# Optimization experiments

Measured on AMD Instinct MI355X. Metric: run time of the kernel, lower is better.

## Reference

```python
import jax, jax.numpy as jnp
from jax import lax
import numpy as np

INPUT_POINTS = 4096
NUM_STAGES = 4
EMBED_DIM = 72
K_NEIGHBORS = 90
ALPHA = 1000.0
BETA = 100.0
B = 4
EPS = 1e-5


def pos_embed(coords, out_dim):
    """coords: [B, Cin, *rest] -> [B, out_dim, *rest].
    Matches PosE_Initial/PosE_Geo: sin/cos interleaved along the feature axis."""
    Bsz, cin = coords.shape[0], coords.shape[1]
    rest = coords.shape[2:]
    feat_dim = out_dim // (cin * 2)
    dim_embed = ALPHA ** (jnp.arange(feat_dim, dtype=coords.dtype) / feat_dim)
    div = BETA * coords[..., None] / dim_embed                 # [B,Cin,*rest,f]
    emb = jnp.stack([jnp.sin(div), jnp.cos(div)], axis=-1)      # [B,Cin,*rest,f,2]
    emb = emb.reshape(coords.shape + (2 * feat_dim,))           # interleave sin/cos
    emb = jnp.moveaxis(emb, -1, 2)                              # [B,Cin,2f,*rest]
    return emb.reshape((Bsz, out_dim) + rest)


def fps(points, n):
    """Farthest point sampling, deterministic start at index 0. points [N,3]."""
    d0 = jnp.full(points.shape[0], jnp.inf, dtype=points.dtype)

    def step(carry, _):
        d, last = carry
        dist = jnp.sum((points - points[last]) ** 2, axis=-1)
        d = jnp.minimum(d, dist)
        return (d, jnp.argmax(d)), last

    _, idx = lax.scan(step, (d0, jnp.argmax(jnp.zeros(points.shape[0]))), None, length=n)
    return idx


def gather_points(points, idx):
    # points [B,N,C], idx [B,...] -> [B,...,C]
    return jax.vmap(lambda p, i: p[i])(points, idx)


def knn_indices(xyz, new_xyz, k):
    # squared pairwise distances [B,S,N] then k smallest
    sq = (jnp.sum(new_xyz ** 2, -1)[:, :, None]
          + jnp.sum(xyz ** 2, -1)[:, None, :]
          - 2.0 * jnp.einsum('bsc,bnc->bsn', new_xyz, xyz))
    _, idx = lax.top_k(-sq, k)
    return idx


def stage(xyz, x, group_num, out_dim, gamma, beta_p):
    # xyz [B,N,3], x [B,N,C]
    fi = fps(xyz[0], group_num)                 # shared across batch (fps with batch=None)
    lc_xyz = xyz[:, fi]                         # [B,G,3]
    lc_x = x[:, fi]                             # [B,G,C]
    ki = knn_indices(xyz, lc_xyz, K_NEIGHBORS)  # [B,G,K]
    knn_xyz = gather_points(xyz, ki)            # [B,G,K,3]
    knn_x = gather_points(x, ki)                # [B,G,K,C]
    # LGA: global scalar std (unbiased, like torch.std) normalization
    dx = knn_x - lc_x[:, :, None, :]
    dxyz = knn_xyz - lc_xyz[:, :, None, :]
    knn_xn = dx / (jnp.std(dx, ddof=1) + EPS)
    knn_xyzn = dxyz / (jnp.std(dxyz, ddof=1) + EPS)
    feat = jnp.concatenate(
        [knn_xn, jnp.broadcast_to(lc_x[:, :, None, :], knn_xn.shape)], axis=-1)
    feat = jnp.transpose(feat, (0, 3, 1, 2))                    # [B,out,G,K]
    pe = pos_embed(jnp.transpose(knn_xyzn, (0, 3, 1, 2)), out_dim)
    w = (feat + pe) * pe                                        # [B,out,G,K]
    # Pooling: max+mean over K, BatchNorm1d (training stats), exact GELU
    lc = jnp.max(w, -1) + jnp.mean(w, -1)                       # [B,out,G]
    mu = jnp.mean(lc, axis=(0, 2), keepdims=True)
    var = jnp.var(lc, axis=(0, 2), keepdims=True)
    lc = (lc - mu) / jnp.sqrt(var + EPS) * gamma[None, :, None] + beta_p[None, :, None]
    return lc_xyz, jax.nn.gelu(lc, approximate=False)


def forward(xyz, x, gammas, betas):
    feat = pos_embed(x, EMBED_DIM)              # [B,72,N]
    out_dim = EMBED_DIM
    group = INPUT_POINTS
    for i in range(NUM_STAGES):
        out_dim *= 2
        group //= 2
        xyz, feat = stage(xyz, jnp.transpose(feat, (0, 2, 1)),
                          group, out_dim, gammas[i], betas[i])
    return jnp.max(feat, -1) + jnp.mean(feat, -1)


def setup_inputs() -> dict:
    key = jax.random.key(0)
    k1, k2 = jax.random.split(key)
    inp = {
        'xyz': jax.random.normal(k1, (B, INPUT_POINTS, 3), jnp.float32),
        'x': jax.random.normal(k2, (B, 3, INPUT_POINTS), jnp.float32),
    }
    dims = [EMBED_DIM * 2 ** (i + 1) for i in range(NUM_STAGES)]
    for i, d in enumerate(dims):
        inp[f'gamma{i}'] = jnp.ones((d,), jnp.float32)
        inp[f'beta{i}'] = jnp.zeros((d,), jnp.float32)
    return inp


def reference(xyz, x, gamma0, beta0, gamma1, beta1, gamma2, beta2, gamma3, beta3):
    return forward(xyz, x,
                   [gamma0, gamma1, gamma2, gamma3],
                   [beta0, beta1, beta2, beta3])
```

## Files before the change

### kernel.cpp

```cpp
#include <hip/hip_runtime.h>

typedef unsigned int u32;
typedef unsigned long long u64;
typedef float v2f __attribute__((ext_vector_type(2)));

#define BB 4
#define NP0 4096
#define KNB 90
#define CC0 72
#define MAXD 1152
#define NSTRIPE 16

__global__ void k_init(const float* __restrict__ xyz, const float* __restrict__ x,
                       float* __restrict__ xs, float* __restrict__ ys, float* __restrict__ zs,
                       float* __restrict__ feat, float* __restrict__ sums){
  int i = blockIdx.x*blockDim.x + threadIdx.x;
  if (i < 16) sums[i] = 0.f;
  if (i < BB*NP0){
    xs[i] = xyz[3*i+0];
    ys[i] = xyz[3*i+1];
    zs[i] = xyz[3*i+2];
  }
  if (i < BB*NP0*36){
    int j = i % 36; int bn = i / 36;
    int n = bn % NP0, b = bn / NP0;
    int cin = j / 12, f = j % 12;
    float xv = x[(b*3+cin)*NP0 + n];
    float rcp = __powf(1000.0f, -(float)f / 12.0f);
    float a = (100.0f * xv) * rcp;
    float sn, cs; __sincosf(a, &sn, &cs);
    float2 v = make_float2(sn, cs);
    *(float2*)(feat + (size_t)bn*CC0 + cin*24 + 2*f) = v;
  }
}

__device__ __forceinline__ void wave_argmax(float bd, int bi, float &smax, int &wbi){
  float v = bd;
  #define DPP_MAX(ctrl) do{ int _t = __builtin_amdgcn_mov_dpp(__float_as_int(v), (ctrl), 0xf, 0xf, true); \
                            v = fmaxf(v, __int_as_float(_t)); }while(0)
  DPP_MAX(0x111); DPP_MAX(0x112); DPP_MAX(0x114); DPP_MAX(0x118);
  DPP_MAX(0x142); DPP_MAX(0x143);
  #undef DPP_MAX
  smax = __int_as_float(__builtin_amdgcn_readlane(__float_as_int(v), 63));
  u64 msk = __ballot(bd == smax);
  int winlane = (int)__ffsll((long long)msk) - 1;
  wbi = __builtin_amdgcn_readlane(bi, winlane);
}

template<int PPT>
__global__ __launch_bounds__(256)
void k_fps4(const float* __restrict__ xs, const float* __restrict__ ys, const float* __restrict__ zs,
            int N, int G, int* __restrict__ fi,
            float* __restrict__ nxs, float* __restrict__ nys, float* __restrict__ nzs){
  constexpr int PH = PPT/2;
  __shared__ float4 sp[4096];
  __shared__ int sfi[2048];
  __shared__ u64 cand[2][4];
  int tid = threadIdx.x;
  const int base = tid * PPT;
  int wv = tid >> 6;
  int lane = tid & 63;
  v2f px[PH], py[PH], pz[PH], dmn[PH];
  #pragma unroll
  for (int j=0;j<PH;j++){
    int n = base + 2*j;
    float2 ax = *(const float2*)(xs+n);
    float2 ay = *(const float2*)(ys+n);
    float2 az = *(const float2*)(zs+n);
    px[j] = (v2f){ax.x, ax.y};
    py[j] = (v2f){ay.x, ay.y};
    pz[j] = (v2f){az.x, az.y};
    sp[n]   = make_float4(ax.x, ay.x, az.x, 0.f);
    sp[n+1] = make_float4(ax.y, ay.y, az.y, 0.f);
    dmn[j] = (v2f){INFINITY, INFINITY};
  }
  if (tid==0){ sfi[0]=0; }
  float lx = xs[0], ly = ys[0], lz = zs[0];
  __syncthreads();
  for (int t=1; t<G; t++){
    float bd = -INFINITY; int bi = base;
    v2f lx2 = (v2f){lx,lx}, ly2 = (v2f){ly,ly}, lz2 = (v2f){lz,lz};
    {
      #pragma clang fp contract(off)
      #pragma unroll
      for (int j=0;j<PH;j++){
        v2f dx = px[j] - lx2;
        v2f dy = py[j] - ly2;
        v2f dz = pz[j] - lz2;
        v2f d2 = (dx*dx + dy*dy) + dz*dz;
        v2f dmo = dmn[j];
        float dm0 = fminf(dmo.x, d2.x);
        float dm1 = fminf(dmo.y, d2.y);
        dmn[j] = (v2f){dm0, dm1};
        bool g0 = dm0 > bd;
        bd = g0 ? dm0 : bd;
        bi = g0 ? (base + 2*j) : bi;
        bool g1 = dm1 > bd;
        bd = g1 ? dm1 : bd;
        bi = g1 ? (base + 2*j + 1) : bi;
      }
    }
    float smax; int wbi;
    wave_argmax(bd, bi, smax, wbi);
    int par = t & 1;
    if (lane == 0) cand[par][wv] = ((u64)__float_as_uint(smax) << 32) | (u32)(~(u32)wbi);
    __syncthreads();
    u64 k0 = cand[par][0], k1 = cand[par][1], k2 = cand[par][2], k3 = cand[par][3];
    u64 ka = k0 > k1 ? k0 : k1;
    u64 kb = k2 > k3 ? k2 : k3;
    u64 km = ka > kb ? ka : kb;
    int w = (int)(~(u32)km);
    if ((u32)w >= (u32)N) w = 0;
    float4 p = sp[w];
    lx = p.x; ly = p.y; lz = p.z;
    if (tid==0){ sfi[t] = w; }
  }
  __syncthreads();
  for (int i = tid; i < G; i += 256) fi[i] = sfi[i];
  for (int i = tid; i < BB*G; i += 256){
    int b = i / G, g = i % G;
    int idx = sfi[g];
    nxs[i] = xs[(size_t)b*N + idx];
    nys[i] = ys[(size_t)b*N + idx];
    nzs[i] = zs[(size_t)b*N + idx];
  }
}

__device__ float blockReduceSum(float v, float* sRed){
  for (int off=32; off; off>>=1) v += __shfl_down(v, off, 64);
  int wid = threadIdx.x >> 6, lane = threadIdx.x & 63;
  __syncthreads();
  if (lane==0) sRed[wid] = v;
  __syncthreads();
  float r = 0;
  if (threadIdx.x == 0){ for (int i=0;i<4;i++) r += sRed[i]; }
  return r;
}

template<int C, int NF>
__global__ __launch_bounds__(256)
void k_knnstd(const float* __restrict__ x,
              const float* __restrict__ xs, const float* __restrict__ ys, const float* __restrict__ zs,
              const float* __restrict__ nxs, const float* __restrict__ nys, const float* __restrict__ nzs,
              const int* __restrict__ fi, int N, int G,
              int* __restrict__ ki, float* __restrict__ sums,
              int* __restrict__ fi2, float* __restrict__ n2xs,
              float* __restrict__ n2ys, float* __restrict__ n2zs){
  extern __shared__ u32 smk[];
  __shared__ u64 candF[2][4];
  int tid = threadIdx.x;
  if constexpr (NF > 0){
    if (blockIdx.x == 0){
      constexpr int PPT = NF/256;
      constexpr int PH = PPT/2;
      constexpr int G2 = NF/2;
      float4* sp = (float4*)smk;
      int* sfi = ((int*)smk) + NF*4;
      const int base = tid * PPT;
      int wv = tid >> 6, lane = tid & 63;
      v2f px[PH], py[PH], pz[PH], dmn[PH];
      #pragma unroll
      for (int j=0;j<PH;j++){
        int n = base + 2*j;
        float2 ax = *(const float2*)(nxs+n);
        float2 ay = *(const float2*)(nys+n);
        float2 az = *(const float2*)(nzs+n);
        px[j] = (v2f){ax.x, ax.y};
        py[j] = (v2f){ay.x, ay.y};
        pz[j] = (v2f){az.x, az.y};
        sp[n]   = make_float4(ax.x, ay.x, az.x, 0.f);
        sp[n+1] = make_float4(ax.y, ay.y, az.y, 0.f);
        dmn[j] = (v2f){INFINITY, INFINITY};
      }
      if (tid==0){ sfi[0]=0; }
      float lx = nxs[0], ly = nys[0], lz = nzs[0];
      __syncthreads();
      for (int t=1; t<G2; t++){
        float bd = -INFINITY; int bi = base;
        v2f lx2 = (v2f){lx,lx}, ly2 = (v2f){ly,ly}, lz2 = (v2f){lz,lz};
        {
          #pragma clang fp contract(off)
          #pragma unroll
          for (int j=0;j<PH;j++){
            v2f dx = px[j] - lx2;
            v2f dy = py[j] - ly2;
            v2f dz = pz[j] - lz2;
            v2f d2 = (dx*dx + dy*dy) + dz*dz;
            v2f dmo = dmn[j];
            float dm0 = fminf(dmo.x, d2.x);
            float dm1 = fminf(dmo.y, d2.y);
            dmn[j] = (v2f){dm0, dm1};
            bool g0 = dm0 > bd;
            bd = g0 ? dm0 : bd;
            bi = g0 ? (base + 2*j) : bi;
            bool g1 = dm1 > bd;
            bd = g1 ? dm1 : bd;
            bi = g1 ? (base + 2*j + 1) : bi;
          }
        }
        float smax; int wbi;
        wave_argmax(bd, bi, smax, wbi);
        int par = t & 1;
        if (lane == 0) candF[par][wv] = ((u64)__float_as_uint(smax) << 32) | (u32)(~(u32)wbi);
        __syncthreads();
        u64 k0 = candF[par][0], k1 = candF[par][1], k2 = candF[par][2], k3 = candF[par][3];
        u64 ka = k0 > k1 ? k0 : k1;
        u64 kb = k2 > k3 ? k2 : k3;
        u64 km = ka > kb ? ka : kb;
        int w = (int)(~(u32)km);
        if ((u32)w >= (u32)NF) w = 0;
        float4 p = sp[w];
        lx = p.x; ly = p.y; lz = p.z;
        if (tid==0){ sfi[t] = w; }
      }
      __syncthreads();
      for (int i = tid; i < G2; i += 256) fi2[i] = sfi[i];
      for (int i = tid; i < BB*G2; i += 256){
        int b2 = i / G2, g2 = i % G2;
        int idx = sfi[g2];
        n2xs[i] = nxs[(size_t)b2*G + idx];
        n2ys[i] = nys[(size_t)b2*G + idx];
        n2zs[i] = nzs[(size_t)b2*G + idx];
      }
      return;
    }
  }
  u32* keys = smk;
  u32* hist = smk + N;
  u32* eq   = hist + 256;
  u32* sc   = eq + 512;
  u32* wtot = sc + 4;
  __shared__ float sLcx[C];
  __shared__ int sKi[KNB];
  __shared__ int sFi;
  __shared__ float sRed[4];
  int bid = (NF > 0) ? ((int)blockIdx.x - 1) : (int)blockIdx.x;
  int wv = tid >> 6, lane = tid & 63;
  int g = bid % G, b = bid / G;
  if (tid==0){ int f0 = fi[g]; if ((u32)f0 >= (u32)N) f0 = 0; sFi = f0; }
  float cx = nxs[b*G+g], cy = nys[b*G+g], cz = nzs[b*G+g];
  float ss = __fadd_rn(__fadd_rn(__fmul_rn(cx,cx), __fmul_rn(cy,cy)), __fmul_rn(cz,cz));
  for (int n = tid; n < N; n += 256){
    float px = xs[b*N+n], py = ys[b*N+n], pz = zs[b*N+n];
    float nn  = __fadd_rn(__fadd_rn(__fmul_rn(px,px), __fmul_rn(py,py)), __fmul_rn(pz,pz));
    float dot = __fadd_rn(__fadd_rn(__fmul_rn(cx,px), __fmul_rn(cy,py)), __fmul_rn(cz,pz));
    float sq  = __fsub_rn(__fadd_rn(ss, nn), __fmul_rn(2.0f, dot));
    u32 u = __float_as_uint(sq);
    keys[n] = (u & 0x80000000u) ? ~u : (u | 0x80000000u);
  }
  if (tid < 4) sc[tid] = 0;
  __syncthreads();
  for (int c = tid; c < C; c += 256) sLcx[c] = x[(size_t)(b*N + sFi)*C + c];
  u32 prefix = 0, bas = 0;
  for (int pass=0; pass<4; pass++){
    int shift = 24 - 8*pass;
    u32 mask = (pass==0) ? 0u : (0xFFFFFFFFu << (shift+8));
    hist[tid] = 0;
    __syncthreads();
    for (int n = tid; n < N; n += 256){
      u32 k = keys[n];
      if ((k & mask) == (prefix & mask))
        atomicAdd(&hist[(k >> shift) & 255u], 1u);
    }
    __syncthreads();
    u32 h = hist[tid];
    u32 p = h;
    #pragma unroll
    for (int off=1; off<64; off<<=1){
      u32 o = __shfl_up(p, off, 64);
      if (lane >= off) p += o;
    }
    if (lane == 63) wtot[wv] = p;
    __syncthreads();
    u32 ex = p - h;
    for (int w2=0; w2<wv; w2++) ex += wtot[w2];
    if (bas + ex < KNB && bas + ex + h >= KNB){
      sc[0] = prefix | ((u32)tid << shift);
      sc[1] = bas + ex;
    }
    __syncthreads();
    prefix = sc[0]; bas = sc[1];
    __syncthreads();
  }
  u32 T = prefix;
  int needEq = KNB - (int)bas;
  int* out = ki + (size_t)(b*G+g)*KNB;
  for (int n = tid; n < N; n += 256){
    u32 k = keys[n];
    if (k < T){
      u32 p2 = atomicAdd(&sc[2], 1u);
      if (p2 < KNB){ out[p2] = n; sKi[p2] = n; }
    } else if (k == T){
      u32 e = atomicAdd(&sc[3], 1u);
      if (e < 512) eq[e] = (u32)n;
    }
  }
  __syncthreads();
  int m = (int)sc[3]; if (m > 512) m = 512;
  for (int i = tid; i < m; i += 256){
    u32 v = eq[i];
    int r = 0;
    for (int j=0; j<m; j++) r += (eq[j] < v);
    if (r < needEq){
      u32 p2 = atomicAdd(&sc[2], 1u);
      if (p2 < KNB){ out[p2] = (int)v; sKi[p2] = (int)v; }
    }
  }
  __syncthreads();
  if (tid == 0){
    u32 c = sc[2];
    while (c < KNB){ out[c] = 0; sKi[c] = 0; c++; }
  }
  __syncthreads();
  float s1=0, s2=0, s3=0, s4=0;
  constexpr int C2 = C/2;
  for (int u2 = tid; u2 < KNB*C2; u2 += 256){
    int k = u2 / C2; int c = (u2 - k*C2)*2;
    int idx = sKi[k];
    float2 v = *(const float2*)(x + (size_t)(b*N + idx)*C + c);
    float a0 = v.x - sLcx[c];
    float a1 = v.y - sLcx[c+1];
    s1 += a0 + a1; s2 += a0*a0 + a1*a1;
  }
  if (tid < 3){
    for (int k=0;k<KNB;k++){
      int idx = sKi[k];
      float pc = (tid==0 ? xs[b*N+idx] : tid==1 ? ys[b*N+idx] : zs[b*N+idx]);
      float cc = (tid==0 ? cx : tid==1 ? cy : cz);
      float w = pc - cc;
      s3 += w; s4 += w*w;
    }
  }
  float t;
  t = blockReduceSum(s1, sRed); if (tid==0) atomicAdd(&sums[0], t);
  t = blockReduceSum(s2, sRed); if (tid==0) atomicAdd(&sums[1], t);
  t = blockReduceSum(s3, sRed); if (tid==0) atomicAdd(&sums[2], t);
  t = blockReduceSum(s4, sRed); if (tid==0) atomicAdd(&sums[3], t);
}

template<int C>
__global__ void k_feat(const float* __restrict__ x,
            const float* __restrict__ xs, const float* __restrict__ ys, const float* __restrict__ zs,
            const float* __restrict__ nxs, const float* __restrict__ nys, const float* __restrict__ nzs,
            const int* __restrict__ fi, const int* __restrict__ ki, const float* __restrict__ sums,
            double n1, double n2,
            int N, int G, float* __restrict__ lc){
  constexpr int D = 2*C;
  constexpr int D3 = D/3;
  constexpr int FD = C/3;
  __shared__ float sLcx[C];
  __shared__ float sDx[KNB*3];
  __shared__ int sKi[KNB];
  __shared__ int sFi;
  __shared__ float sC[3];
  __shared__ float sInv2[2];
  int tid = threadIdx.x;
  int g = blockIdx.x % G, b = blockIdx.x / G;
  if (tid==0){ int f0 = fi[g]; if ((u32)f0 >= (u32)N) f0 = 0; sFi = f0; }
  if (tid==0){
    double s1 = sums[0], s2 = sums[1];
    double mean = s1/n1;
    double var = (s2 - s1*mean)/(n1 - 1.0); if (var < 0) var = 0;
    sInv2[0] = (float)(1.0/(sqrt(var) + 1e-5));
    double t1 = sums[2], t2 = sums[3];
    double m2 = t1/n2;
    double v2 = (t2 - t1*m2)/(n2 - 1.0); if (v2 < 0) v2 = 0;
    sInv2[1] = (float)(1.0/(sqrt(v2) + 1e-5));
  }
  if (tid<3) sC[tid] = (tid==0 ? nxs[b*G+g] : tid==1 ? nys[b*G+g] : nzs[b*G+g]);
  if (tid < KNB){ int v = ki[(size_t)(b*G+g)*KNB + tid]; if ((u32)v >= (u32)N) v = 0; sKi[tid] = v; }
  __syncthreads();
  for (int c = tid; c < C; c += blockDim.x) sLcx[c] = x[(size_t)(b*N + sFi)*C + c];
  for (int t = tid; t < KNB*3; t += blockDim.x){
    int k = t/3, c = t%3;
    int idx = sKi[k];
    float pc = (c==0 ? xs[b*N+idx] : c==1 ? ys[b*N+idx] : zs[b*N+idx]);
    sDx[t] = (pc - sC[c]) * sInv2[1];
  }
  __syncthreads();
  int p = tid;
  if (p >= C) return;
  int d0 = 2*p;
  int c = d0 / D3;
  int f = (d0 - c*D3) >> 1;
  float rcp = __powf(1000.0f, -(float)f / (float)FD);
  bool low = (d0 < C);
  float invdx = sInv2[0];
  float fh0 = 0.f, fh1 = 0.f;
  if (!low){ fh0 = sLcx[d0-C]; fh1 = sLcx[d0+1-C]; }
  float l0 = low ? sLcx[d0] : 0.f, l1 = low ? sLcx[d0+1] : 0.f;
  float mx0=-INFINITY, mx1=-INFINITY, sm0=0.f, sm1=0.f;
  for (int k=0;k<KNB;k++){
    float a = (100.0f * sDx[k*3+c]) * rcp;
    float sn, cs; __sincosf(a, &sn, &cs);
    float f0, f1;
    if (low){
      float2 v = *(const float2*)(x + (size_t)(b*N + sKi[k])*C + d0);
      f0 = (v.x - l0) * invdx;
      f1 = (v.y - l1) * invdx;
    } else { f0 = fh0; f1 = fh1; }
    float w0 = (f0 + sn)*sn;
    float w1 = (f1 + cs)*cs;
    mx0 = fmaxf(mx0, w0); sm0 += w0;
    mx1 = fmaxf(mx1, w1); sm1 += w1;
  }
  float* o = lc + (size_t)(b*G+g)*D + d0;
  o[0] = mx0 + sm0/90.0f;
  o[1] = mx1 + sm1/90.0f;
}

__global__ __launch_bounds__(256)
void k_bnpart(const float* __restrict__ lc, int D, int M,
              double* __restrict__ PS, double* __restrict__ PQ){
  __shared__ double sS[4][64], sQ[4][64];
  int lane = threadIdx.x & 63, row = threadIdx.x >> 6;
  int tile = blockIdx.x, stripe = blockIdx.y;
  int d = tile*64 + lane;
  int span = M / NSTRIPE;
  int i0 = stripe * span;
  double s=0, q=0;
  if (d < D){
    for (int i=i0+row; i<i0+span; i+=4){
      float v = lc[(size_t)i*D + d];
      s += v; q += (double)v*v;
    }
  }
  sS[row][lane]=s; sQ[row][lane]=q;
  __syncthreads();
  if (row==0 && d < D){
    PS[(size_t)stripe*MAXD + d] = sS[0][lane]+sS[1][lane]+sS[2][lane]+sS[3][lane];
    PQ[(size_t)stripe*MAXD + d] = sQ[0][lane]+sQ[1][lane]+sQ[2][lane]+sQ[3][lane];
  }
}

__global__ void k_bnfin(const double* __restrict__ PS, const double* __restrict__ PQ,
                        const float* __restrict__ gamma, const float* __restrict__ beta,
                        int D, int M, float* __restrict__ A, float* __restrict__ Bb){
  int d = blockIdx.x*64 + threadIdx.x;
  if (d >= D) return;
  double ts=0, tq=0;
  for (int s=0; s<NSTRIPE; s++){ ts += PS[(size_t)s*MAXD + d]; tq += PQ[(size_t)s*MAXD + d]; }
  double mean = ts / M;
  double var = tq / M - mean*mean; if (var < 0) var = 0;
  float rstd = (float)(1.0/sqrt(var + 1e-5));
  float gm = gamma[d], bt = beta[d];
  A[d] = gm*rstd;
  Bb[d] = bt - (float)mean*gm*rstd;
}

__global__ void k_apply(float* __restrict__ lc, const float* __restrict__ A,
                        const float* __restrict__ Bb, int D, int total){
  int i = blockIdx.x*blockDim.x + threadIdx.x;
  if (i >= total) return;
  int d = i % D;
  float v = lc[i]*A[d] + Bb[d];
  lc[i] = 0.5f * v * (1.0f + erff(v * 0.70710678118654752f));
}

__global__ void k_out(const float* __restrict__ feat, float* __restrict__ out){
  int i = blockIdx.x*blockDim.x + threadIdx.x;
  if (i >= BB*1152) return;
  int b = i / 1152, d = i % 1152;
  const float* base = feat + (size_t)b*256*1152 + d;
  float mx = -INFINITY, sm = 0.f;
  for (int g=0; g<256; g++){
    float v = base[(size_t)g*1152];
    mx = fmaxf(mx, v); sm += v;
  }
  out[i] = mx + sm/256.0f;
}

extern "C" void kernel_launch(void* const* d_in, const int* in_sizes, int n_in,
                              void* d_out, int out_size, void* d_ws, size_t ws_size,
                              hipStream_t stream) {
  const float* xyz = (const float*)d_in[0];
  const float* xin = (const float*)d_in[1];
  float* ws = (float*)d_ws;
  size_t off = 0;
  const size_t PS_ = (size_t)BB*NP0;
  const size_t XS = (size_t)BB*NP0*CC0;
  float* T0[3]; float* T1[3]; float* T2[3];
  for (int i=0;i<3;i++){ T0[i] = ws + off; off += PS_; }
  for (int i=0;i<3;i++){ T1[i] = ws + off; off += PS_; }
  for (int i=0;i<3;i++){ T2[i] = ws + off; off += PS_; }
  float* xA = ws + off; off += XS;
  float* xB = ws + off; off += XS;
  int*   fiA = (int*)(ws + off); off += 2048;
  int*   fiB = (int*)(ws + off); off += 2048;
  int*   ki = (int*)(ws + off); off += (size_t)BB*2048*KNB;
  float* sums = ws + off; off += 16;
  float* Abn  = ws + off; off += 1152;
  float* Bbn  = ws + off; off += 1152;
  off = (off + 1) & ~(size_t)1;
  double* PSb = (double*)(ws + off); off += (size_t)NSTRIPE*MAXD*2;
  double* PQb = (double*)(ws + off); off += (size_t)NSTRIPE*MAXD*2;

  k_init<<<(BB*NP0*36+255)/256, 256, 0, stream>>>(xyz, xin, T0[0], T0[1], T0[2], xA, sums);
  k_fps4<16><<<1, 256, 0, stream>>>(T0[0],T0[1],T0[2], NP0, NP0/2, fiA, T1[0],T1[1],T1[2]);

  float **P = T0, **Cn = T1, **Nx = T2;
  int *fiC = fiA, *fiN = fiB;
  float *xc = xA, *lc = xB;
  for (int s=0; s<4; s++){
    int N = NP0 >> s, G = N >> 1, C = CC0 << s, D = 2*C;
    float* ssum = sums + 4*s;
    size_t knn_need = (size_t)(N + 256 + 512 + 8 + 8)*4;
    if (s==0){
      size_t lds = knn_need; size_t fps_need = (size_t)2048*16 + 1024*4;
      if (fps_need > lds) lds = fps_need;
      k_knnstd<72,2048><<<BB*G+1, 256, lds, stream>>>(xc, P[0],P[1],P[2], Cn[0],Cn[1],Cn[2],
          fiC, N, G, ki, ssum, fiN, Nx[0],Nx[1],Nx[2]);
    } else if (s==1){
      size_t lds = knn_need; size_t fps_need = (size_t)1024*16 + 512*4;
      if (fps_need > lds) lds = fps_need;
      k_knnstd<144,1024><<<BB*G+1, 256, lds, stream>>>(xc, P[0],P[1],P[2], Cn[0],Cn[1],Cn[2],
          fiC, N, G, ki, ssum, fiN, Nx[0],Nx[1],Nx[2]);
    } else if (s==2){
      size_t lds = knn_need; size_t fps_need = (size_t)512*16 + 256*4;
      if (fps_need > lds) lds = fps_need;
      k_knnstd<288,512><<<BB*G+1, 256, lds, stream>>>(xc, P[0],P[1],P[2], Cn[0],Cn[1],Cn[2],
          fiC, N, G, ki, ssum, fiN, Nx[0],Nx[1],Nx[2]);
    } else {
      k_knnstd<576,0><<<BB*G, 256, knn_need, stream>>>(xc, P[0],P[1],P[2], Cn[0],Cn[1],Cn[2],
          fiC, N, G, ki, ssum, nullptr, nullptr, nullptr, nullptr);
    }
    double n1 = (double)BB*G*KNB*C, n2 = (double)BB*G*KNB*3;
    int Tp = ((C + 63)/64)*64;
    if (s==0)      k_feat<72 ><<<BB*G, Tp, 0, stream>>>(xc, P[0],P[1],P[2], Cn[0],Cn[1],Cn[2], fiC, ki, ssum, n1, n2, N, G, lc);
    else if (s==1) k_feat<144><<<BB*G, Tp, 0, stream>>>(xc, P[0],P[1],P[2], Cn[0],Cn[1],Cn[2], fiC, ki, ssum, n1, n2, N, G, lc);
    else if (s==2) k_feat<288><<<BB*G, Tp, 0, stream>>>(xc, P[0],P[1],P[2], Cn[0],Cn[1],Cn[2], fiC, ki, ssum, n1, n2, N, G, lc);
    else           k_feat<576><<<BB*G, Tp, 0, stream>>>(xc, P[0],P[1],P[2], Cn[0],Cn[1],Cn[2], fiC, ki, ssum, n1, n2, N, G, lc);
    int M = BB*G;
    dim3 bng((D + 63)/64, NSTRIPE);
    k_bnpart<<<bng, 256, 0, stream>>>(lc, D, M, PSb, PQb);
    k_bnfin<<<(D + 63)/64, 64, 0, stream>>>(PSb, PQb, (const float*)d_in[2+2*s],
                                            (const float*)d_in[3+2*s], D, M, Abn, Bbn);
    int total = M*D;
    k_apply<<<(total+255)/256, 256, 0, stream>>>(lc, Abn, Bbn, D, total);
    float** t = P; P = Cn; Cn = Nx; Nx = t;
    int* ti = fiC; fiC = fiN; fiN = ti;
    float* tf = xc; xc = lc; lc = tf;
  }
  k_out<<<(BB*1152+255)/256, 256, 0, stream>>>(xc, (float*)d_out);
}
```

Baseline: 2.488 ms.

## Split next-stage FPS across knn and feat kernels with spilled state

Measured after the change: 2.633 ms. 1.06x slower.

```diff
diff --git a/kernel.cpp b/kernel.cpp
--- a/kernel.cpp
+++ b/kernel.cpp
@@ -10,6 +10,7 @@
 #define CC0 72
 #define MAXD 1152
 #define NSTRIPE 16
+#define FSPLIT 700
 
 __global__ void k_init(const float* __restrict__ xyz, const float* __restrict__ x,
                        float* __restrict__ xs, float* __restrict__ ys, float* __restrict__ zs,
@@ -126,6 +127,108 @@
   }
 }
 
+template<int NF, int NT>
+__device__ __forceinline__
+void fps_chunk(const float* __restrict__ cxs, const float* __restrict__ cys, const float* __restrict__ czs,
+               int t0, int t1,
+               float* __restrict__ dmnG, float4* __restrict__ cenG,
+               int* __restrict__ fi2,
+               float* __restrict__ n2xs, float* __restrict__ n2ys, float* __restrict__ n2zs,
+               u64 (&cand)[2][4]){
+  constexpr int PPT = NF/NT;
+  constexpr int PH = PPT/2;
+  constexpr int G2 = NF/2;
+  constexpr int NW = NT/64;
+  int tid = threadIdx.x;
+  const int base = tid * PPT;
+  int wv = tid >> 6, lane = tid & 63;
+  v2f px[PH], py[PH], pz[PH], dmn[PH];
+  #pragma unroll
+  for (int j=0;j<PH;j++){
+    int n = base + 2*j;
+    float2 ax = *(const float2*)(cxs+n);
+    float2 ay = *(const float2*)(cys+n);
+    float2 az = *(const float2*)(czs+n);
+    px[j] = (v2f){ax.x, ax.y};
+    py[j] = (v2f){ay.x, ay.y};
+    pz[j] = (v2f){az.x, az.y};
+  }
+  float lx, ly, lz;
+  if (t0 == 1){
+    #pragma unroll
+    for (int j=0;j<PH;j++) dmn[j] = (v2f){INFINITY, INFINITY};
+    if (tid==0) fi2[0] = 0;
+    lx = cxs[0]; ly = cys[0]; lz = czs[0];
+  } else {
+    #pragma unroll
+    for (int j=0;j<PH;j++){
+      float2 dv = *(const float2*)(dmnG + base + 2*j);
+      dmn[j] = (v2f){dv.x, dv.y};
+    }
+    float4 c = *cenG;
+    lx = c.x; ly = c.y; lz = c.z;
+  }
+  for (int t=t0; t<t1; t++){
+    float bd = -INFINITY; int bi = base;
+    v2f lx2 = (v2f){lx,lx}, ly2 = (v2f){ly,ly}, lz2 = (v2f){lz,lz};
+    {
+      #pragma clang fp contract(off)
+      #pragma unroll
+      for (int j=0;j<PH;j++){
+        v2f dx = px[j] - lx2;
+        v2f dy = py[j] - ly2;
+        v2f dz = pz[j] - lz2;
+        v2f d2 = (dx*dx + dy*dy) + dz*dz;
+        v2f dmo = dmn[j];
+        float dm0 = fminf(dmo.x, d2.x);
+        float dm1 = fminf(dmo.y, d2.y);
+        dmn[j] = (v2f){dm0, dm1};
+        bool g0 = dm0 > bd;
+        bd = g0 ? dm0 : bd;
+        bi = g0 ? (base + 2*j) : bi;
+        bool g1 = dm1 > bd;
+        bd = g1 ? dm1 : bd;
+        bi = g1 ? (base + 2*j + 1) : bi;
+      }
+    }
+    float smax; int wbi;
+    wave_argmax(bd, bi, smax, wbi);
+    int par = t & 1;
+    if (lane == 0) cand[par][wv] = ((u64)__float_as_uint(smax) << 32) | (u32)(~(u32)wbi);
+    __syncthreads();
+    u64 km;
+    if constexpr (NW == 4){
+      u64 k0 = cand[par][0], k1 = cand[par][1], k2 = cand[par][2], k3 = cand[par][3];
+      u64 ka = k0 > k1 ? k0 : k1;
+      u64 kb = k2 > k3 ? k2 : k3;
+      km = ka > kb ? ka : kb;
+    } else {
+      u64 k0 = cand[par][0], k1 = cand[par][1];
+      km = k0 > k1 ? k0 : k1;
+    }
+    int w = (int)(~(u32)km);
+    if ((u32)w >= (u32)NF) w = 0;
+    lx = cxs[w]; ly = cys[w]; lz = czs[w];
+    if (tid==0) fi2[t] = w;
+  }
+  if (t1 < G2){
+    #pragma unroll
+    for (int j=0;j<PH;j++)
+      *(float2*)(dmnG + base + 2*j) = make_float2(dmn[j].x, dmn[j].y);
+    if (tid==0) *cenG = make_float4(lx, ly, lz, 0.f);
+  } else {
+    __syncthreads();
+    for (int i = tid; i < BB*G2; i += NT){
+      int b2 = i / G2, g2 = i % G2;
+      int idx = fi2[g2];
+      if ((u32)idx >= (u32)NF) idx = 0;
+      n2xs[i] = cxs[(size_t)b2*NF + idx];
+      n2ys[i] = cys[(size_t)b2*NF + idx];
+      n2zs[i] = czs[(size_t)b2*NF + idx];
+    }
+  }
+}
+
 __device__ float blockReduceSum(float v, float* sRed){
   for (int off=32; off; off>>=1) v += __shfl_down(v, off, 64);
   int wid = threadIdx.x >> 6, lane = threadIdx.x & 63;
@@ -144,6 +247,7 @@
               const float* __restrict__ nxs, const float* __restrict__ nys, const float* __restrict__ nzs,
               const int* __restrict__ fi, int N, int G,
               int* __restrict__ ki, float* __restrict__ sums,
+              int t0, int t1, float* __restrict__ dmnG, float4* __restrict__ cenG,
               int* __restrict__ fi2, float* __restrict__ n2xs,
               float* __restrict__ n2ys, float* __restrict__ n2zs){
   extern __shared__ u32 smk[];
@@ -151,77 +255,7 @@
   int tid = threadIdx.x;
   if constexpr (NF > 0){
     if (blockIdx.x == 0){
-      constexpr int PPT = NF/256;
-      constexpr int PH = PPT/2;
-      constexpr int G2 = NF/2;
-      float4* sp = (float4*)smk;
-      int* sfi = ((int*)smk) + NF*4;
-      const int base = tid * PPT;
-      int wv = tid >> 6, lane = tid & 63;
-      v2f px[PH], py[PH], pz[PH], dmn[PH];
-      #pragma unroll
-      for (int j=0;j<PH;j++){
-        int n = base + 2*j;
-        float2 ax = *(const float2*)(nxs+n);
-        float2 ay = *(const float2*)(nys+n);
-        float2 az = *(const float2*)(nzs+n);
-        px[j] = (v2f){ax.x, ax.y};
-        py[j] = (v2f){ay.x, ay.y};
-        pz[j] = (v2f){az.x, az.y};
-        sp[n]   = make_float4(ax.x, ay.x, az.x, 0.f);
-        sp[n+1] = make_float4(ax.y, ay.y, az.y, 0.f);
-        dmn[j] = (v2f){INFINITY, INFINITY};
-      }
-      if (tid==0){ sfi[0]=0; }
-      float lx = nxs[0], ly = nys[0], lz = nzs[0];
-      __syncthreads();
-      for (int t=1; t<G2; t++){
-        float bd = -INFINITY; int bi = base;
-        v2f lx2 = (v2f){lx,lx}, ly2 = (v2f){ly,ly}, lz2 = (v2f){lz,lz};
-        {
-          #pragma clang fp contract(off)
-          #pragma unroll
-          for (int j=0;j<PH;j++){
-            v2f dx = px[j] - lx2;
-            v2f dy = py[j] - ly2;
-            v2f dz = pz[j] - lz2;
-            v2f d2 = (dx*dx + dy*dy) + dz*dz;
-            v2f dmo = dmn[j];
-            float dm0 = fminf(dmo.x, d2.x);
-            float dm1 = fminf(dmo.y, d2.y);
-            dmn[j] = (v2f){dm0, dm1};
-            bool g0 = dm0 > bd;
-            bd = g0 ? dm0 : bd;
-            bi = g0 ? (base + 2*j) : bi;
-            bool g1 = dm1 > bd;
-            bd = g1 ? dm1 : bd;
-            bi = g1 ? (base + 2*j + 1) : bi;
-          }
-        }
-        float smax; int wbi;
-        wave_argmax(bd, bi, smax, wbi);
-        int par = t & 1;
-        if (lane == 0) candF[par][wv] = ((u64)__float_as_uint(smax) << 32) | (u32)(~(u32)wbi);
-        __syncthreads();
-        u64 k0 = candF[par][0], k1 = candF[par][1], k2 = candF[par][2], k3 = candF[par][3];
-        u64 ka = k0 > k1 ? k0 : k1;
-        u64 kb = k2 > k3 ? k2 : k3;
-        u64 km = ka > kb ? ka : kb;
-        int w = (int)(~(u32)km);
-        if ((u32)w >= (u32)NF) w = 0;
-        float4 p = sp[w];
-        lx = p.x; ly = p.y; lz = p.z;
-        if (tid==0){ sfi[t] = w; }
-      }
-      __syncthreads();
-      for (int i = tid; i < G2; i += 256) fi2[i] = sfi[i];
-      for (int i = tid; i < BB*G2; i += 256){
-        int b2 = i / G2, g2 = i % G2;
-        int idx = sfi[g2];
-        n2xs[i] = nxs[(size_t)b2*G + idx];
-        n2ys[i] = nys[(size_t)b2*G + idx];
-        n2zs[i] = nzs[(size_t)b2*G + idx];
-      }
+      fps_chunk<NF,256>(nxs, nys, nzs, t0, t1, dmnG, cenG, fi2, n2xs, n2ys, n2zs, candF);
       return;
     }
   }
@@ -338,16 +372,20 @@
   t = blockReduceSum(s4, sRed); if (tid==0) atomicAdd(&sums[3], t);
 }
 
-template<int C>
+template<int C, int NF, int NT>
 __global__ void k_feat(const float* __restrict__ x,
             const float* __restrict__ xs, const float* __restrict__ ys, const float* __restrict__ zs,
             const float* __restrict__ nxs, const float* __restrict__ nys, const float* __restrict__ nzs,
             const int* __restrict__ fi, const int* __restrict__ ki, const float* __restrict__ sums,
             double n1, double n2,
-            int N, int G, float* __restrict__ lc){
+            int N, int G, float* __restrict__ lc,
+            int t0, int t1, float* __restrict__ dmnG, float4* __restrict__ cenG,
+            int* __restrict__ fi2, float* __restrict__ n2xs,
+            float* __restrict__ n2ys, float* __restrict__ n2zs){
   constexpr int D = 2*C;
   constexpr int D3 = D/3;
   constexpr int FD = C/3;
+  __shared__ u64 candF[2][4];
   __shared__ float sLcx[C];
   __shared__ float sDx[KNB*3];
   __shared__ int sKi[KNB];
@@ -355,16 +393,23 @@
   __shared__ float sC[3];
   __shared__ float sInv2[2];
   int tid = threadIdx.x;
-  int g = blockIdx.x % G, b = blockIdx.x / G;
+  if constexpr (NF > 0){
+    if (blockIdx.x == 0){
+      fps_chunk<NF,NT>(nxs, nys, nzs, t0, t1, dmnG, cenG, fi2, n2xs, n2ys, n2zs, candF);
+      return;
+    }
+  }
+  int bid = (NF > 0) ? ((int)blockIdx.x - 1) : (int)blockIdx.x;
+  int g = bid % G, b = bid / G;
   if (tid==0){ int f0 = fi[g]; if ((u32)f0 >= (u32)N) f0 = 0; sFi = f0; }
   if (tid==0){
     double s1 = sums[0], s2 = sums[1];
     double mean = s1/n1;
     double var = (s2 - s1*mean)/(n1 - 1.0); if (var < 0) var = 0;
     sInv2[0] = (float)(1.0/(sqrt(var) + 1e-5));
-    double t1 = sums[2], t2 = sums[3];
-    double m2 = t1/n2;
-    double v2 = (t2 - t1*m2)/(n2 - 1.0); if (v2 < 0) v2 = 0;
+    double t1d = sums[2], t2d = sums[3];
+    double m2 = t1d/n2;
+    double v2 = (t2d - t1d*m2)/(n2 - 1.0); if (v2 < 0) v2 = 0;
     sInv2[1] = (float)(1.0/(sqrt(v2) + 1e-5));
   }
   if (tid<3) sC[tid] = (tid==0 ? nxs[b*G+g] : tid==1 ? nys[b*G+g] : nzs[b*G+g]);
@@ -491,6 +536,8 @@
   float* sums = ws + off; off += 16;
   float* Abn  = ws + off; off += 1152;
   float* Bbn  = ws + off; off += 1152;
+  float* dmnG = ws + off; off += 2048;
+  float4* cenG = (float4*)(ws + off); off += 4;
   off = (off + 1) & ~(size_t)1;
   double* PSb = (double*)(ws + off); off += (size_t)NSTRIPE*MAXD*2;
   double* PQb = (double*)(ws + off); off += (size_t)NSTRIPE*MAXD*2;
@@ -504,32 +551,35 @@
   for (int s=0; s<4; s++){
     int N = NP0 >> s, G = N >> 1, C = CC0 << s, D = 2*C;
     float* ssum = sums + 4*s;
-    size_t knn_need = (size_t)(N + 256 + 512 + 8 + 8)*4;
+    size_t knn_lds = (size_t)(N + 256 + 512 + 8 + 8)*4;
     if (s==0){
-      size_t lds = knn_need; size_t fps_need = (size_t)2048*16 + 1024*4;
-      if (fps_need > lds) lds = fps_need;
-      k_knnstd<72,2048><<<BB*G+1, 256, lds, stream>>>(xc, P[0],P[1],P[2], Cn[0],Cn[1],Cn[2],
-          fiC, N, G, ki, ssum, fiN, Nx[0],Nx[1],Nx[2]);
+      k_knnstd<72,2048><<<BB*G+1, 256, knn_lds, stream>>>(xc, P[0],P[1],P[2], Cn[0],Cn[1],Cn[2],
+          fiC, N, G, ki, ssum, 1, FSPLIT, dmnG, cenG, fiN, Nx[0],Nx[1],Nx[2]);
     } else if (s==1){
-      size_t lds = knn_need; size_t fps_need = (size_t)1024*16 + 512*4;
-      if (fps_need > lds) lds = fps_need;
-      k_knnstd<144,1024><<<BB*G+1, 256, lds, stream>>>(xc, P[0],P[1],P[2], Cn[0],Cn[1],Cn[2],
-          fiC, N, G, ki, ssum, fiN, Nx[0],Nx[1],Nx[2]);
+      k_knnstd<144,1024><<<BB*G+1, 256, knn_lds, stream>>>(xc, P[0],P[1],P[2], Cn[0],Cn[1],Cn[2],
+          fiC, N, G, ki, ssum, 1, 512, dmnG, cenG, fiN, Nx[0],Nx[1],Nx[2]);
     } else if (s==2){
-      size_t lds = knn_need; size_t fps_need = (size_t)512*16 + 256*4;
-      if (fps_need > lds) lds = fps_need;
-      k_knnstd<288,512><<<BB*G+1, 256, lds, stream>>>(xc, P[0],P[1],P[2], Cn[0],Cn[1],Cn[2],
-          fiC, N, G, ki, ssum, fiN, Nx[0],Nx[1],Nx[2]);
+      k_knnstd<288,512><<<BB*G+1, 256, knn_lds, stream>>>(xc, P[0],P[1],P[2], Cn[0],Cn[1],Cn[2],
+          fiC, N, G, ki, ssum, 1, 256, dmnG, cenG, fiN, Nx[0],Nx[1],Nx[2]);
     } else {
-      k_knnstd<576,0><<<BB*G, 256, knn_need, stream>>>(xc, P[0],P[1],P[2], Cn[0],Cn[1],Cn[2],
-          fiC, N, G, ki, ssum, nullptr, nullptr, nullptr, nullptr);
+      k_knnstd<576,0><<<BB*G, 256, knn_lds, stream>>>(xc, P[0],P[1],P[2], Cn[0],Cn[1],Cn[2],
+          fiC, N, G, ki, ssum, 0, 0, nullptr, nullptr, nullptr, nullptr, nullptr, nullptr);
     }
     double n1 = (double)BB*G*KNB*C, n2 = (double)BB*G*KNB*3;
     int Tp = ((C + 63)/64)*64;
-    if (s==0)      k_feat<72 ><<<BB*G, Tp, 0, stream>>>(xc, P[0],P[1],P[2], Cn[0],Cn[1],Cn[2], fiC, ki, ssum, n1, n2, N, G, lc);
-    else if (s==1) k_feat<144><<<BB*G, Tp, 0, stream>>>(xc, P[0],P[1],P[2], Cn[0],Cn[1],Cn[2], fiC, ki, ssum, n1, n2, N, G, lc);
-    else if (s==2) k_feat<288><<<BB*G, Tp, 0, stream>>>(xc, P[0],P[1],P[2], Cn[0],Cn[1],Cn[2], fiC, ki, ssum, n1, n2, N, G, lc);
-    else           k_feat<576><<<BB*G, Tp, 0, stream>>>(xc, P[0],P[1],P[2], Cn[0],Cn[1],Cn[2], fiC, ki, ssum, n1, n2, N, G, lc);
+    if (s==0){
+      k_feat<72,2048,128><<<BB*G+1, Tp, 0, stream>>>(xc, P[0],P[1],P[2], Cn[0],Cn[1],Cn[2], fiC, ki, ssum,
+          n1, n2, N, G, lc, FSPLIT, 1024, dmnG, cenG, fiN, Nx[0],Nx[1],Nx[2]);
+    } else if (s==1){
+      k_feat<144,0,0><<<BB*G, Tp, 0, stream>>>(xc, P[0],P[1],P[2], Cn[0],Cn[1],Cn[2], fiC, ki, ssum,
+          n1, n2, N, G, lc, 0, 0, nullptr, nullptr, nullptr, nullptr, nullptr, nullptr);
+    } else if (s==2){
+      k_feat<288,0,0><<<BB*G, Tp, 0, stream>>>(xc, P[0],P[1],P[2], Cn[0],Cn[1],Cn[2], fiC, ki, ssum,
+          n1, n2, N, G, lc, 0, 0, nullptr, nullptr, nullptr, nullptr, nullptr, nullptr);
+    } else {
+      k_feat<576,0,0><<<BB*G, Tp, 0, stream>>>(xc, P[0],P[1],P[2], Cn[0],Cn[1],Cn[2], fiC, ki, ssum,
+          n1, n2, N, G, lc, 0, 0, nullptr, nullptr, nullptr, nullptr, nullptr, nullptr);
+    }
     int M = BB*G;
     dim3 bng((D + 63)/64, NSTRIPE);
     k_bnpart<<<bng, 256, 0, stream>>>(lc, D, M, PSb, PQb);
```
